# Optimization experiments

Measured on AMD Instinct MI355X. Metric: run time of the kernel, lower is better.

Reference implementation:

```python
import jax, jax.numpy as jnp
import numpy as np

HEAD_NUM = 16
HEAD_DIM = 64
INPUT_DIM = 1024
OUTPUT_DIM = 1024
NEG_INF = -1e9  # value the torch code writes into masked score positions


def setup_inputs() -> dict:
    key = jax.random.key(0)
    k_x, k_v, k_w1, k_b1, k_w2, k_b2 = jax.random.split(key, 6)
    B, N = 2, 2048
    x = jax.random.normal(k_x, (B, N, INPUT_DIM), dtype=jnp.float32)
    vaild_num = jax.random.randint(k_v, (B,), 0, N, dtype=jnp.int32)
    s1 = 1.0 / np.sqrt(INPUT_DIM)
    s2 = 1.0 / np.sqrt(HEAD_NUM * HEAD_DIM)
    W_qkv = jax.random.uniform(k_w1, (INPUT_DIM, 3 * HEAD_NUM * HEAD_DIM), jnp.float32, -s1, s1)
    b_qkv = jax.random.uniform(k_b1, (3 * HEAD_NUM * HEAD_DIM,), jnp.float32, -s1, s1)
    W_proj = jax.random.uniform(k_w2, (HEAD_NUM * HEAD_DIM, OUTPUT_DIM), jnp.float32, -s2, s2)
    b_proj = jax.random.uniform(k_b2, (OUTPUT_DIM,), jnp.float32, -s2, s2)
    return {"x": x, "vaild_num": vaild_num, "W_qkv": W_qkv, "b_qkv": b_qkv,
            "W_proj": W_proj, "b_proj": b_proj}


def reference(x, vaild_num, W_qkv, b_qkv, W_proj, b_proj):
    B, N, _ = x.shape
    H, hd = HEAD_NUM, HEAD_DIM
    qkv = x @ W_qkv + b_qkv                      # [B, N, 3*H*hd]
    q, k, v = jnp.split(qkv, 3, axis=2)
    split = lambda t: t.reshape(B, N, H, hd).transpose(0, 2, 1, 3)  # [B, H, N, hd]
    q, k, v = split(q), split(k), split(v)
    score = jnp.einsum('bhqd,bhkd->bhqk', q, k) * (1.0 / np.sqrt(hd))
    # per-sample valid-length masking: rows >= v and cols >= v get -1e9
    valid = jnp.arange(N)[None, :] < vaild_num[:, None]            # [B, N]
    mask = valid[:, None, :, None] & valid[:, None, None, :]       # [B, 1, N, N]
    score = jnp.where(mask, score, NEG_INF)
    p = jax.nn.softmax(score, axis=-1)
    attn = jnp.einsum('bhqk,bhkd->bhqd', p, v)                     # [B, H, N, hd]
    attn = attn.transpose(0, 2, 1, 3).reshape(B, N, H * hd)
    return attn @ W_proj + b_proj
```

## Files before the change

### kernel.cpp

```cpp
#include <hip/hip_runtime.h>
#include <stdint.h>


typedef float    f32x4  __attribute__((ext_vector_type(4)));
typedef float    f32x16 __attribute__((ext_vector_type(16)));
typedef __bf16   bf16x8 __attribute__((ext_vector_type(8)));
typedef unsigned short u16x8 __attribute__((ext_vector_type(8)));
typedef unsigned int   u32x4 __attribute__((ext_vector_type(4)));
typedef unsigned short ushort_t;
typedef unsigned int   u32;

#define HEADS 16
#define HDIM  64
#define NTOK  2048
#define BATCH 2
#define DIN   1024
#define D3    3072
#define MTOT  4096

#define SC 0.18033688f

__device__ __forceinline__ ushort_t f2bf(float x) {
  uint32_t u = __builtin_bit_cast(uint32_t, x);
  uint32_t r = (u + 0x7fffu + ((u >> 16) & 1u)) >> 16;
  return (ushort_t)r;
}
__device__ __forceinline__ float bf2f(ushort_t u) {
  return __builtin_bit_cast(float, (uint32_t)u << 16);
}
__device__ __forceinline__ u32 cvt_pk_bf16(float lo, float hi) {
  u32 r;
  asm("v_cvt_pk_bf16_f32 %0, %1, %2" : "=v"(r) : "v"(lo), "v"(hi));
  return r;
}

__device__ __forceinline__ void gld_lds16(const void* g, void* l) {
  auto gp = reinterpret_cast<const __attribute__((address_space(1))) uint32_t*>(
      reinterpret_cast<uintptr_t>(g));
  auto lp = reinterpret_cast<__attribute__((address_space(3))) uint32_t*>(
      reinterpret_cast<uintptr_t>(l));
  __builtin_amdgcn_global_load_lds(gp, lp, 16, 0, 0);
}

__device__ __forceinline__ void transpose_tile(
    const float* __restrict__ in, ushort_t* __restrict__ out,
    int R, int C, int bx, int by, float (*tile)[65]) {
  const int r0 = by * 64, c0 = bx * 64;
  const int t = threadIdx.x;
#pragma unroll
  for (int it = 0; it < 4; ++it) {
    int r = it * 16 + (t >> 4);
    int c = (t & 15) * 4;
    float4 v = *(const float4*)(in + (size_t)(r0 + r) * C + c0 + c);
    tile[r][c] = v.x; tile[r][c+1] = v.y; tile[r][c+2] = v.z; tile[r][c+3] = v.w;
  }
  __syncthreads();
#pragma unroll
  for (int it = 0; it < 2; ++it) {
    int idx = it * 2048 + t * 8;
    int c = idx >> 6;
    int r = idx & 63;
    u16x8 v;
#pragma unroll
    for (int j = 0; j < 8; ++j) v[j] = f2bf(tile[r + j][c]);
    *(u16x8*)(out + (size_t)(c0 + c) * R + r0 + r) = v;
  }
}

__global__ __launch_bounds__(256) void prep_kernel(
    const float* __restrict__ x, ushort_t* __restrict__ xb,
    const float* __restrict__ Wq, ushort_t* __restrict__ wqT,
    const float* __restrict__ Wp, ushort_t* __restrict__ wpT) {
  __shared__ float tile[64][65];
  const int bid = blockIdx.x;
  if (bid < 2048) {
    const int i = (bid * 256 + threadIdx.x) * 8;
    float4 a = *(const float4*)(x + i);
    float4 b = *(const float4*)(x + i + 4);
    u16x8 v;
    v[0]=f2bf(a.x); v[1]=f2bf(a.y); v[2]=f2bf(a.z); v[3]=f2bf(a.w);
    v[4]=f2bf(b.x); v[5]=f2bf(b.y); v[6]=f2bf(b.z); v[7]=f2bf(b.w);
    *(u16x8*)(xb + i) = v;
  } else if (bid < 2816) {
    const int idx = bid - 2048;
    transpose_tile(Wq, wqT, 1024, 3072, idx % 48, idx / 48, tile);
  } else {
    const int idx = bid - 2816;
    transpose_tile(Wp, wpT, 1024, 1024, idx % 16, idx / 16, tile);
  }
}

template <bool SWAP>
__device__ __forceinline__ void gemm_tile_mainloop(
    const ushort_t* __restrict__ A, const ushort_t* __restrict__ Bt,
    const int K, const int m0, const int n0,
    ushort_t* aT, ushort_t* bT, f32x4 (&acc)[4][4]) {
  const int t = threadIdx.x;
  const int l = t & 63;
  const int wr = t >> 7;
  const int wc = (t >> 6) & 1;

#pragma unroll
  for (int mi = 0; mi < 4; ++mi)
#pragma unroll
    for (int ni = 0; ni < 4; ++ni) acc[mi][ni] = f32x4{0.f, 0.f, 0.f, 0.f};

  for (int k0 = 0; k0 < K; k0 += 64) {
#pragma unroll
    for (int c = 0; c < 4; ++c) {
      const int lin = c * 4096 + t * 16;
      const int row = lin >> 7;
      const int scb = (lin & 127) ^ ((row & 7) << 4);
      const int ldso = (c * 4096 + (t >> 6) * 1024) >> 1;
      gld_lds16(A + (size_t)(m0 + row) * K + k0 + (scb >> 1), aT + ldso);
      gld_lds16(Bt + (size_t)(n0 + row) * K + k0 + (scb >> 1), bT + ldso);
    }
    __syncthreads();
#pragma unroll
    for (int ks = 0; ks < 2; ++ks) {
      bf16x8 af[4], bfr[4];
#pragma unroll
      for (int mi = 0; mi < 4; ++mi) {
        const int row = wr * 64 + mi * 16 + (l & 15);
        const int cb = (((l >> 4) << 4) + (ks << 6)) ^ ((row & 7) << 4);
        af[mi] = *(const bf16x8*)((const char*)aT + row * 128 + cb);
      }
#pragma unroll
      for (int ni = 0; ni < 4; ++ni) {
        const int row = wc * 64 + ni * 16 + (l & 15);
        const int cb = (((l >> 4) << 4) + (ks << 6)) ^ ((row & 7) << 4);
        bfr[ni] = *(const bf16x8*)((const char*)bT + row * 128 + cb);
      }
#pragma unroll
      for (int mi = 0; mi < 4; ++mi)
#pragma unroll
        for (int ni = 0; ni < 4; ++ni) {
          if (SWAP)
            acc[mi][ni] = __builtin_amdgcn_mfma_f32_16x16x32_bf16(
                bfr[ni], af[mi], acc[mi][ni], 0, 0, 0);
          else
            acc[mi][ni] = __builtin_amdgcn_mfma_f32_16x16x32_bf16(
                af[mi], bfr[ni], acc[mi][ni], 0, 0, 0);
        }
    }
    __syncthreads();
  }
}

__global__ __launch_bounds__(256) void gemm_qkv_kernel(
    const ushort_t* __restrict__ xb, const ushort_t* __restrict__ wT,
    const float* __restrict__ bias,
    ushort_t* __restrict__ Qb, ushort_t* __restrict__ Kb, ushort_t* __restrict__ Vt) {
  __shared__ __align__(16) ushort_t aT[128 * 64];
  __shared__ __align__(16) ushort_t bT[128 * 64];
  f32x4 acc[4][4];
  const int m0 = blockIdx.y * 128, n0 = blockIdx.x * 128;
  const int which = n0 >> 10;

  const int t = threadIdx.x, l = t & 63;
  const int wr = t >> 7, wc = (t >> 6) & 1;

  if (which != 2) {
    gemm_tile_mainloop<false>(xb, wT, DIN, m0, n0, aT, bT, acc);
#pragma unroll
    for (int mi = 0; mi < 4; ++mi) {
#pragma unroll
      for (int ni = 0; ni < 4; ++ni) {
        const int n = n0 + wc * 64 + ni * 16 + (l & 15);
        const int h = (n >> 6) & 15, d = n & 63;
        const float bv = bias[n];
#pragma unroll
        for (int i = 0; i < 4; ++i) {
          const int m = m0 + wr * 64 + mi * 16 + ((l >> 4) << 2) + i;
          const int b = m >> 11, tok = m & 2047;
          const ushort_t val = f2bf(acc[mi][ni][i] + bv);
          const size_t bh = (size_t)((b << 4) + h);
          if (which == 0) Qb[(bh * NTOK + tok) * HDIM + d] = val;
          else            Kb[(bh * NTOK + tok) * HDIM + d] = val;
        }
      }
    }
  } else {
    gemm_tile_mainloop<true>(xb, wT, DIN, m0, n0, aT, bT, acc);
    const int b = m0 >> 11;
    const int tok_base = (m0 & 2047) + wr * 64 + (l & 15);
    const int nd_base = (n0 - 2048) + wc * 64 + ((l >> 4) << 2);
#pragma unroll
    for (int mi = 0; mi < 4; ++mi) {
      const int tok = tok_base + mi * 16;
#pragma unroll
      for (int ni = 0; ni < 4; ++ni) {
#pragma unroll
        for (int i = 0; i < 4; ++i) {
          const int nd = nd_base + ni * 16 + i;
          const int h = nd >> 6, d = nd & 63;
          const float bv = bias[2048 + nd];
          Vt[(((size_t)((b << 4) + h) << 6) + d) * NTOK + tok] =
              f2bf(acc[mi][ni][i] + bv);
        }
      }
    }
  }
}

__global__ __launch_bounds__(256) void gemm_proj_kernel(
    const ushort_t* __restrict__ ab, const ushort_t* __restrict__ wT,
    const float* __restrict__ bias, float* __restrict__ out) {
  __shared__ __align__(16) ushort_t aT[128 * 64];
  __shared__ __align__(16) ushort_t bT[128 * 64];
  f32x4 acc[4][4];
  const int m0 = blockIdx.y * 128, n0 = blockIdx.x * 128;
  gemm_tile_mainloop<false>(ab, wT, DIN, m0, n0, aT, bT, acc);

  const int t = threadIdx.x, l = t & 63;
  const int wr = t >> 7, wc = (t >> 6) & 1;
#pragma unroll
  for (int mi = 0; mi < 4; ++mi) {
#pragma unroll
    for (int ni = 0; ni < 4; ++ni) {
      const int n = n0 + wc * 64 + ni * 16 + (l & 15);
      const float bv = bias[n];
#pragma unroll
      for (int i = 0; i < 4; ++i) {
        const int m = m0 + wr * 64 + mi * 16 + ((l >> 4) << 2) + i;
        out[(size_t)m * 1024 + n] = acc[mi][ni][i] + bv;
      }
    }
  }
}

__global__ __launch_bounds__(256) void vmean_kernel(
    const ushort_t* __restrict__ Vt, ushort_t* __restrict__ vmean) {
  const int row = blockIdx.x * 4 + (threadIdx.x >> 6);
  const int l = threadIdx.x & 63;
  const ushort_t* src = Vt + (size_t)row * NTOK;
  float s = 0.f;
#pragma unroll
  for (int j = 0; j < 4; ++j) {
    u16x8 v = *(const u16x8*)(src + ((j << 6) + l) * 8);
#pragma unroll
    for (int k = 0; k < 8; ++k) s += bf2f(v[k]);
  }
#pragma unroll
  for (int d2 = 1; d2 < 64; d2 <<= 1) s += __shfl_xor(s, d2);
  if (l == 0) vmean[row] = f2bf(s * (1.0f / 2048.0f));
}

__global__ __launch_bounds__(256) void attn_kernel(
    const ushort_t* __restrict__ Qb, const ushort_t* __restrict__ Kb,
    const ushort_t* __restrict__ Vt, const ushort_t* __restrict__ vmean,
    const int* __restrict__ validp, ushort_t* __restrict__ ob) {
  __shared__ __align__(16) char smem_raw[65536];

  const int h = blockIdx.y, b = blockIdx.z;
  const int valid = validp[b];
  const int t = threadIdx.x, w = t >> 6, l = t & 63;
  const int lq = l & 31, hi = l >> 5;
  const int bq0 = blockIdx.x << 7;
  const int wq0 = bq0 + (w << 5);
  const size_t bh = (size_t)((b << 4) + h);
  const ushort_t* Qp = Qb + bh * (NTOK * HDIM);
  const ushort_t* Kp = Kb + bh * (NTOK * HDIM);
  const ushort_t* Vp = Vt + bh * (HDIM * NTOK);

  f32x16 oacc[2];
#pragma unroll
  for (int db = 0; db < 2; ++db)
#pragma unroll
    for (int r = 0; r < 16; ++r) oacc[db][r] = 0.f;
  float m_run = -INFINITY, lsum = 0.f;

  if (bq0 < valid) {
    const bool qvalid = (wq0 < valid);
    bf16x8 qf[4];
    if (qvalid) {
      const ushort_t* qbase = Qp + (size_t)(wq0 + lq) * HDIM + (hi << 3);
#pragma unroll
      for (int ks = 0; ks < 4; ++ks) qf[ks] = *(const bf16x8*)(qbase + (ks << 4));
    }

    const int nt = (valid + 127) >> 7;

    auto STAGE = [&](int p, int kv0) {
      char* kdst = smem_raw + p * 32768;
      char* vdst = kdst + 16384;
#pragma unroll
      for (int c = 0; c < 4; ++c) {
        const int lin = c * 4096 + t * 16;
        const int ldso = c * 4096 + (w << 10);
        {
          const int row = lin >> 7;
          const int scb = (lin & 127) ^ ((row & 7) << 4);
          gld_lds16(Kp + (size_t)(kv0 + row) * HDIM + (scb >> 1), kdst + ldso);
        }
        {
          const int row = lin >> 8;
          const int scb = (lin & 255) ^ ((row & 7) << 4);
          gld_lds16(Vp + (size_t)row * NTOK + kv0 + (scb >> 1), vdst + ldso);
        }
      }
    };

    STAGE(0, 0);
    asm volatile("s_waitcnt vmcnt(0)" ::: "memory");
    __builtin_amdgcn_s_barrier();

    for (int tt = 0; tt < nt; ++tt) {
      const int p = tt & 1;
      const int kv0 = tt << 7;
      if (tt + 1 < nt) {
        STAGE(p ^ 1, (tt + 1) << 7);
        asm volatile("s_waitcnt vmcnt(8)" ::: "memory");
      } else {
        asm volatile("s_waitcnt vmcnt(0)" ::: "memory");
      }
      __builtin_amdgcn_sched_barrier(0);
      __builtin_amdgcn_s_barrier();

      if (qvalid) {
        const char* kbuf = smem_raw + p * 32768;
        const char* vbuf = kbuf + 16384;

        bf16x8 kf[4][4];
#pragma unroll
        for (int kb2 = 0; kb2 < 4; ++kb2) {
          const int row = (kb2 << 5) + lq;
          const int sw = (row & 7) << 4;
#pragma unroll
          for (int ks = 0; ks < 4; ++ks)
            kf[kb2][ks] = *(const bf16x8*)(kbuf + row * 128 + (((ks << 5) + (hi << 4)) ^ sw));
        }

        f32x16 st[4];
#pragma unroll
        for (int kb2 = 0; kb2 < 4; ++kb2)
#pragma unroll
          for (int r = 0; r < 16; ++r) st[kb2][r] = 0.f;
        __builtin_amdgcn_s_setprio(1);
#pragma unroll
        for (int ks = 0; ks < 4; ++ks) {
          st[0] = __builtin_amdgcn_mfma_f32_32x32x16_bf16(kf[0][ks], qf[ks], st[0], 0, 0, 0);
          st[1] = __builtin_amdgcn_mfma_f32_32x32x16_bf16(kf[1][ks], qf[ks], st[1], 0, 0, 0);
          st[2] = __builtin_amdgcn_mfma_f32_32x32x16_bf16(kf[2][ks], qf[ks], st[2], 0, 0, 0);
          st[3] = __builtin_amdgcn_mfma_f32_32x32x16_bf16(kf[3][ks], qf[ks], st[3], 0, 0, 0);
        }
        __builtin_amdgcn_s_setprio(0);

        if (kv0 + 128 > valid) {
#pragma unroll
          for (int kb2 = 0; kb2 < 4; ++kb2)
#pragma unroll
            for (int r = 0; r < 16; ++r) {
              const int k = kv0 + (kb2 << 5) + (r & 3) + ((r >> 2) << 3) + (hi << 2);
              if (k >= valid) st[kb2][r] = -1e30f;
            }
        }

        float pm;
        {
          float a8[8];
#pragma unroll
          for (int i = 0; i < 8; ++i)
            a8[i] = fmaxf(fmaxf(fmaxf(st[0][i], st[0][i + 8]), fmaxf(st[1][i], st[1][i + 8])),
                          fmaxf(fmaxf(st[2][i], st[2][i + 8]), fmaxf(st[3][i], st[3][i + 8])));
          float b4[4];
#pragma unroll
          for (int i = 0; i < 4; ++i) b4[i] = fmaxf(a8[i], a8[i + 4]);
          pm = fmaxf(fmaxf(b4[0], b4[1]), fmaxf(b4[2], b4[3]));
        }
        pm = fmaxf(pm, __shfl_xor(pm, 32));

        if (__any(pm > m_run)) {
          const float mnew = fmaxf(m_run, pm);
          const float rs = exp2f((m_run - mnew) * SC);
          lsum *= rs;
#pragma unroll
          for (int db = 0; db < 2; ++db)
#pragma unroll
            for (int r = 0; r < 16; ++r) oacc[db][r] *= rs;
          m_run = mnew;
        }

        const float mc = m_run * SC;
        float pp[4][16];
        float ts4[4] = {0.f, 0.f, 0.f, 0.f};
#pragma unroll
        for (int kb2 = 0; kb2 < 4; ++kb2)
#pragma unroll
          for (int r = 0; r < 16; ++r) {
            const float e = exp2f(fmaf(st[kb2][r], SC, -mc));
            pp[kb2][r] = e;
            ts4[r & 3] += e;
          }
        float tsum = (ts4[0] + ts4[1]) + (ts4[2] + ts4[3]);
        tsum += __shfl_xor(tsum, 32);
        lsum += tsum;

        bf16x8 pb[4][2];
#pragma unroll
        for (int kb2 = 0; kb2 < 4; ++kb2) {
          u32 c[8];
#pragma unroll
          for (int m2 = 0; m2 < 8; ++m2)
            c[m2] = cvt_pk_bf16(pp[kb2][2 * m2], pp[kb2][2 * m2 + 1]);
          const u32 x1 = (u32)__shfl_xor((int)(hi ? c[0] : c[2]), 32);
          const u32 x2 = (u32)__shfl_xor((int)(hi ? c[1] : c[3]), 32);
          const u32 x3 = (u32)__shfl_xor((int)(hi ? c[4] : c[6]), 32);
          const u32 x4 = (u32)__shfl_xor((int)(hi ? c[5] : c[7]), 32);
          u32x4 w0, w1;
          w0[0] = hi ? x1 : c[0];  w0[1] = hi ? x2 : c[1];
          w0[2] = hi ? c[2] : x1;  w0[3] = hi ? c[3] : x2;
          w1[0] = hi ? x3 : c[4];  w1[1] = hi ? x4 : c[5];
          w1[2] = hi ? c[6] : x3;  w1[3] = hi ? c[7] : x4;
          pb[kb2][0] = __builtin_bit_cast(bf16x8, w0);
          pb[kb2][1] = __builtin_bit_cast(bf16x8, w1);
        }

        __builtin_amdgcn_s_setprio(1);
#pragma unroll
        for (int db = 0; db < 2; ++db) {
          const int row = (db << 5) + lq;
          const int sw = (row & 7) << 4;
#pragma unroll
          for (int ksl = 0; ksl < 8; ++ksl) {
            const bf16x8 vf = *(const bf16x8*)(vbuf + row * 256 + (((ksl << 5) + (hi << 4)) ^ sw));
            oacc[db] = __builtin_amdgcn_mfma_f32_32x32x16_bf16(
                vf, pb[ksl >> 1][ksl & 1], oacc[db], 0, 0, 0);
          }
        }
        __builtin_amdgcn_s_setprio(0);
      }

      __builtin_amdgcn_s_barrier();
    }
  }

  const float inv = (lsum > 0.f) ? 1.0f / lsum : 0.f;
  ushort_t* ot = (ushort_t*)smem_raw + w * (32 * 68);
#pragma unroll
  for (int db = 0; db < 2; ++db)
#pragma unroll
    for (int r = 0; r < 16; ++r) {
      const int d = (r & 3) + ((r >> 2) << 3) + (hi << 2) + (db << 5);
      ot[lq * 68 + d] = f2bf(oacc[db][r] * inv);
    }
  asm volatile("s_waitcnt lgkmcnt(0)" ::: "memory");
#pragma unroll
  for (int it = 0; it < 8; ++it) {
    const int c2 = it * 64 + l;
    const int row = c2 >> 4;
    const int ch = c2 & 15;
    const uint2 vo = *(const uint2*)((const char*)ot + row * 136 + ch * 8);
    const uint2 vm = *(const uint2*)(vmean + (bh << 6) + ch * 4);
    const int grow = bq0 + (w << 5) + row;
    const uint2 sel = (grow < valid) ? vo : vm;
    *(uint2*)(ob + ((size_t)(b * NTOK) + grow) * 1024 + (h << 6) + ch * 4) = sel;
  }
}

extern "C" void kernel_launch(void* const* d_in, const int* in_sizes, int n_in,
                              void* d_out, int out_size, void* d_ws, size_t ws_size,
                              hipStream_t stream) {
  (void)in_sizes; (void)n_in; (void)out_size; (void)ws_size;
  const float* x      = (const float*)d_in[0];
  const int*   validp = (const int*)d_in[1];
  const float* W_qkv  = (const float*)d_in[2];
  const float* b_qkv  = (const float*)d_in[3];
  const float* W_proj = (const float*)d_in[4];
  const float* b_proj = (const float*)d_in[5];
  float* out = (float*)d_out;

  ushort_t* xb     = (ushort_t*)d_ws;
  ushort_t* wqkvT  = xb + 4194304;
  ushort_t* wprojT = wqkvT + 3145728;
  ushort_t* Qb     = wprojT + 1048576;
  ushort_t* Kb     = Qb + 4194304;
  ushort_t* Vt     = Kb + 4194304;
  ushort_t* ab     = Vt + 4194304;
  ushort_t* vm     = ab + 4194304;

  prep_kernel<<<3072, 256, 0, stream>>>(x, xb, W_qkv, wqkvT, W_proj, wprojT);
  gemm_qkv_kernel<<<dim3(24, 32), 256, 0, stream>>>(xb, wqkvT, b_qkv, Qb, Kb, Vt);
  vmean_kernel<<<512, 256, 0, stream>>>(Vt, vm);
  attn_kernel<<<dim3(16, 16, 2), 256, 0, stream>>>(Qb, Kb, Vt, vm, validp, ab);
  gemm_proj_kernel<<<dim3(8, 32), 256, 0, stream>>>(ab, wprojT, b_proj, out);
}
```

Baseline: 206.7 us.

## Split attention KV range across two blocks and merge partial results

The attention kernel now launches twice as many blocks. Each block processes alternating 128-key tiles (split-K, flash-decoding style) and writes bf16 partial outputs plus per-row max and sum to workspace. A new merge kernel combines the two partials with log-sum-exp rescaling and fills invalid rows with the V mean. This raises parallelism and occupancy for the attention stage, which had only 512 blocks with uneven valid lengths. The cost is an extra kernel launch, extra memory traffic for the partials, and bf16 rounding of the intermediate outputs.

```diff
diff --git a/kernel.cpp b/kernel.cpp
--- a/kernel.cpp
+++ b/kernel.cpp
@@ -248,21 +248,25 @@
 
 __global__ __launch_bounds__(256) void attn_kernel(
     const ushort_t* __restrict__ Qb, const ushort_t* __restrict__ Kb,
-    const ushort_t* __restrict__ Vt, const ushort_t* __restrict__ vmean,
-    const int* __restrict__ validp, ushort_t* __restrict__ ob) {
+    const ushort_t* __restrict__ Vt, const int* __restrict__ validp,
+    ushort_t* __restrict__ pO, float* __restrict__ pML) {
   __shared__ __align__(16) char smem_raw[65536];
 
+  const int qt = blockIdx.x & 15, half = blockIdx.x >> 4;
   const int h = blockIdx.y, b = blockIdx.z;
   const int valid = validp[b];
   const int t = threadIdx.x, w = t >> 6, l = t & 63;
   const int lq = l & 31, hi = l >> 5;
-  const int bq0 = blockIdx.x << 7;
+  const int bq0 = qt << 7;
   const int wq0 = bq0 + (w << 5);
   const size_t bh = (size_t)((b << 4) + h);
+  const int pidx = (int)((bh << 4) + qt) * 2 + half;
   const ushort_t* Qp = Qb + bh * (NTOK * HDIM);
   const ushort_t* Kp = Kb + bh * (NTOK * HDIM);
   const ushort_t* Vp = Vt + bh * (HDIM * NTOK);
 
+  if (bq0 >= valid) return;
+
   f32x16 oacc[2];
 #pragma unroll
   for (int db = 0; db < 2; ++db)
@@ -270,169 +274,170 @@
     for (int r = 0; r < 16; ++r) oacc[db][r] = 0.f;
   float m_run = -INFINITY, lsum = 0.f;
 
-  if (bq0 < valid) {
-    const bool qvalid = (wq0 < valid);
-    bf16x8 qf[4];
-    if (qvalid) {
-      const ushort_t* qbase = Qp + (size_t)(wq0 + lq) * HDIM + (hi << 3);
-#pragma unroll
-      for (int ks = 0; ks < 4; ++ks) qf[ks] = *(const bf16x8*)(qbase + (ks << 4));
-    }
-
-    const int nt = (valid + 127) >> 7;
-
-    auto STAGE = [&](int p, int kv0) {
-      char* kdst = smem_raw + p * 32768;
-      char* vdst = kdst + 16384;
-#pragma unroll
-      for (int c = 0; c < 4; ++c) {
-        const int lin = c * 4096 + t * 16;
-        const int ldso = c * 4096 + (w << 10);
-        {
-          const int row = lin >> 7;
-          const int scb = (lin & 127) ^ ((row & 7) << 4);
-          gld_lds16(Kp + (size_t)(kv0 + row) * HDIM + (scb >> 1), kdst + ldso);
-        }
-        {
-          const int row = lin >> 8;
-          const int scb = (lin & 255) ^ ((row & 7) << 4);
-          gld_lds16(Vp + (size_t)row * NTOK + kv0 + (scb >> 1), vdst + ldso);
-        }
-      }
-    };
-
-    STAGE(0, 0);
+  const bool qvalid = (wq0 < valid);
+  bf16x8 qf[4];
+  if (qvalid) {
+    const ushort_t* qbase = Qp + (size_t)(wq0 + lq) * HDIM + (hi << 3);
+#pragma unroll
+    for (int ks = 0; ks < 4; ++ks) qf[ks] = *(const bf16x8*)(qbase + (ks << 4));
+  }
+
+  const int nt = (valid + 127) >> 7;
+  const int ntb = (nt - half + 1) >> 1;
+
+  auto STAGE = [&](int p, int kv0) {
+    char* kdst = smem_raw + p * 32768;
+    char* vdst = kdst + 16384;
+#pragma unroll
+    for (int c = 0; c < 4; ++c) {
+      const int lin = c * 4096 + t * 16;
+      const int ldso = c * 4096 + (w << 10);
+      {
+        const int row = lin >> 7;
+        const int scb = (lin & 127) ^ ((row & 7) << 4);
+        gld_lds16(Kp + (size_t)(kv0 + row) * HDIM + (scb >> 1), kdst + ldso);
+      }
+      {
+        const int row = lin >> 8;
+        const int scb = (lin & 255) ^ ((row & 7) << 4);
+        gld_lds16(Vp + (size_t)row * NTOK + kv0 + (scb >> 1), vdst + ldso);
+      }
+    }
+  };
+
+  if (ntb > 0) {
+    STAGE(0, half << 7);
     asm volatile("s_waitcnt vmcnt(0)" ::: "memory");
     __builtin_amdgcn_s_barrier();
-
-    for (int tt = 0; tt < nt; ++tt) {
-      const int p = tt & 1;
-      const int kv0 = tt << 7;
-      if (tt + 1 < nt) {
-        STAGE(p ^ 1, (tt + 1) << 7);
-        asm volatile("s_waitcnt vmcnt(8)" ::: "memory");
-      } else {
-        asm volatile("s_waitcnt vmcnt(0)" ::: "memory");
-      }
-      __builtin_amdgcn_sched_barrier(0);
-      __builtin_amdgcn_s_barrier();
-
-      if (qvalid) {
-        const char* kbuf = smem_raw + p * 32768;
-        const char* vbuf = kbuf + 16384;
-
-        bf16x8 kf[4][4];
-#pragma unroll
-        for (int kb2 = 0; kb2 < 4; ++kb2) {
-          const int row = (kb2 << 5) + lq;
-          const int sw = (row & 7) << 4;
-#pragma unroll
-          for (int ks = 0; ks < 4; ++ks)
-            kf[kb2][ks] = *(const bf16x8*)(kbuf + row * 128 + (((ks << 5) + (hi << 4)) ^ sw));
+  }
+
+  for (int j = 0; j < ntb; ++j) {
+    const int p = j & 1;
+    const int kv0 = (half + 2 * j) << 7;
+    if (j + 1 < ntb) {
+      STAGE(p ^ 1, (half + 2 * (j + 1)) << 7);
+      asm volatile("s_waitcnt vmcnt(8)" ::: "memory");
+    } else {
+      asm volatile("s_waitcnt vmcnt(0)" ::: "memory");
+    }
+    __builtin_amdgcn_sched_barrier(0);
+    __builtin_amdgcn_s_barrier();
+
+    if (qvalid) {
+      const char* kbuf = smem_raw + p * 32768;
+      const char* vbuf = kbuf + 16384;
+
+      bf16x8 kf[4][4];
+#pragma unroll
+      for (int kb2 = 0; kb2 < 4; ++kb2) {
+        const int row = (kb2 << 5) + lq;
+        const int sw = (row & 7) << 4;
+#pragma unroll
+        for (int ks = 0; ks < 4; ++ks)
+          kf[kb2][ks] = *(const bf16x8*)(kbuf + row * 128 + (((ks << 5) + (hi << 4)) ^ sw));
+      }
+
+      f32x16 st[4];
+#pragma unroll
+      for (int kb2 = 0; kb2 < 4; ++kb2)
+#pragma unroll
+        for (int r = 0; r < 16; ++r) st[kb2][r] = 0.f;
+      __builtin_amdgcn_s_setprio(1);
+#pragma unroll
+      for (int ks = 0; ks < 4; ++ks) {
+        st[0] = __builtin_amdgcn_mfma_f32_32x32x16_bf16(kf[0][ks], qf[ks], st[0], 0, 0, 0);
+        st[1] = __builtin_amdgcn_mfma_f32_32x32x16_bf16(kf[1][ks], qf[ks], st[1], 0, 0, 0);
+        st[2] = __builtin_amdgcn_mfma_f32_32x32x16_bf16(kf[2][ks], qf[ks], st[2], 0, 0, 0);
+        st[3] = __builtin_amdgcn_mfma_f32_32x32x16_bf16(kf[3][ks], qf[ks], st[3], 0, 0, 0);
+      }
+      __builtin_amdgcn_s_setprio(0);
+
+      if (kv0 + 128 > valid) {
+#pragma unroll
+        for (int kb2 = 0; kb2 < 4; ++kb2)
+#pragma unroll
+          for (int r = 0; r < 16; ++r) {
+            const int k = kv0 + (kb2 << 5) + (r & 3) + ((r >> 2) << 3) + (hi << 2);
+            if (k >= valid) st[kb2][r] = -1e30f;
+          }
+      }
+
+      float pm;
+      {
+        float a8[8];
+#pragma unroll
+        for (int i = 0; i < 8; ++i)
+          a8[i] = fmaxf(fmaxf(fmaxf(st[0][i], st[0][i + 8]), fmaxf(st[1][i], st[1][i + 8])),
+                        fmaxf(fmaxf(st[2][i], st[2][i + 8]), fmaxf(st[3][i], st[3][i + 8])));
+        float b4[4];
+#pragma unroll
+        for (int i = 0; i < 4; ++i) b4[i] = fmaxf(a8[i], a8[i + 4]);
+        pm = fmaxf(fmaxf(b4[0], b4[1]), fmaxf(b4[2], b4[3]));
+      }
+      pm = fmaxf(pm, __shfl_xor(pm, 32));
+
+      if (__any(pm > m_run)) {
+        const float mnew = fmaxf(m_run, pm);
+        const float rs = exp2f((m_run - mnew) * SC);
+        lsum *= rs;
+#pragma unroll
+        for (int db = 0; db < 2; ++db)
+#pragma unroll
+          for (int r = 0; r < 16; ++r) oacc[db][r] *= rs;
+        m_run = mnew;
+      }
+
+      const float mc = m_run * SC;
+      float pp[4][16];
+      float ts4[4] = {0.f, 0.f, 0.f, 0.f};
+#pragma unroll
+      for (int kb2 = 0; kb2 < 4; ++kb2)
+#pragma unroll
+        for (int r = 0; r < 16; ++r) {
+          const float e = exp2f(fmaf(st[kb2][r], SC, -mc));
+          pp[kb2][r] = e;
+          ts4[r & 3] += e;
         }
-
-        f32x16 st[4];
-#pragma unroll
-        for (int kb2 = 0; kb2 < 4; ++kb2)
-#pragma unroll
-          for (int r = 0; r < 16; ++r) st[kb2][r] = 0.f;
-        __builtin_amdgcn_s_setprio(1);
-#pragma unroll
-        for (int ks = 0; ks < 4; ++ks) {
-          st[0] = __builtin_amdgcn_mfma_f32_32x32x16_bf16(kf[0][ks], qf[ks], st[0], 0, 0, 0);
-          st[1] = __builtin_amdgcn_mfma_f32_32x32x16_bf16(kf[1][ks], qf[ks], st[1], 0, 0, 0);
-          st[2] = __builtin_amdgcn_mfma_f32_32x32x16_bf16(kf[2][ks], qf[ks], st[2], 0, 0, 0);
-          st[3] = __builtin_amdgcn_mfma_f32_32x32x16_bf16(kf[3][ks], qf[ks], st[3], 0, 0, 0);
+      float tsum = (ts4[0] + ts4[1]) + (ts4[2] + ts4[3]);
+      tsum += __shfl_xor(tsum, 32);
+      lsum += tsum;
+
+      bf16x8 pb[4][2];
+#pragma unroll
+      for (int kb2 = 0; kb2 < 4; ++kb2) {
+        u32 c[8];
+#pragma unroll
+        for (int m2 = 0; m2 < 8; ++m2)
+          c[m2] = cvt_pk_bf16(pp[kb2][2 * m2], pp[kb2][2 * m2 + 1]);
+        const u32 x1 = (u32)__shfl_xor((int)(hi ? c[0] : c[2]), 32);
+        const u32 x2 = (u32)__shfl_xor((int)(hi ? c[1] : c[3]), 32);
+        const u32 x3 = (u32)__shfl_xor((int)(hi ? c[4] : c[6]), 32);
+        const u32 x4 = (u32)__shfl_xor((int)(hi ? c[5] : c[7]), 32);
+        u32x4 w0, w1;
+        w0[0] = hi ? x1 : c[0];  w0[1] = hi ? x2 : c[1];
+        w0[2] = hi ? c[2] : x1;  w0[3] = hi ? c[3] : x2;
+        w1[0] = hi ? x3 : c[4];  w1[1] = hi ? x4 : c[5];
+        w1[2] = hi ? c[6] : x3;  w1[3] = hi ? c[7] : x4;
+        pb[kb2][0] = __builtin_bit_cast(bf16x8, w0);
+        pb[kb2][1] = __builtin_bit_cast(bf16x8, w1);
+      }
+
+      __builtin_amdgcn_s_setprio(1);
+#pragma unroll
+      for (int db = 0; db < 2; ++db) {
+        const int row = (db << 5) + lq;
+        const int sw = (row & 7) << 4;
+#pragma unroll
+        for (int ksl = 0; ksl < 8; ++ksl) {
+          const bf16x8 vf = *(const bf16x8*)(vbuf + row * 256 + (((ksl << 5) + (hi << 4)) ^ sw));
+          oacc[db] = __builtin_amdgcn_mfma_f32_32x32x16_bf16(
+              vf, pb[ksl >> 1][ksl & 1], oacc[db], 0, 0, 0);
         }
-        __builtin_amdgcn_s_setprio(0);
-
-        if (kv0 + 128 > valid) {
-#pragma unroll
-          for (int kb2 = 0; kb2 < 4; ++kb2)
-#pragma unroll
-            for (int r = 0; r < 16; ++r) {
-              const int k = kv0 + (kb2 << 5) + (r & 3) + ((r >> 2) << 3) + (hi << 2);
-              if (k >= valid) st[kb2][r] = -1e30f;
-            }
-        }
-
-        float pm;
-        {
-          float a8[8];
-#pragma unroll
-          for (int i = 0; i < 8; ++i)
-            a8[i] = fmaxf(fmaxf(fmaxf(st[0][i], st[0][i + 8]), fmaxf(st[1][i], st[1][i + 8])),
-                          fmaxf(fmaxf(st[2][i], st[2][i + 8]), fmaxf(st[3][i], st[3][i + 8])));
-          float b4[4];
-#pragma unroll
-          for (int i = 0; i < 4; ++i) b4[i] = fmaxf(a8[i], a8[i + 4]);
-          pm = fmaxf(fmaxf(b4[0], b4[1]), fmaxf(b4[2], b4[3]));
-        }
-        pm = fmaxf(pm, __shfl_xor(pm, 32));
-
-        if (__any(pm > m_run)) {
-          const float mnew = fmaxf(m_run, pm);
-          const float rs = exp2f((m_run - mnew) * SC);
-          lsum *= rs;
-#pragma unroll
-          for (int db = 0; db < 2; ++db)
-#pragma unroll
-            for (int r = 0; r < 16; ++r) oacc[db][r] *= rs;
-          m_run = mnew;
-        }
-
-        const float mc = m_run * SC;
-        float pp[4][16];
-        float ts4[4] = {0.f, 0.f, 0.f, 0.f};
-#pragma unroll
-        for (int kb2 = 0; kb2 < 4; ++kb2)
-#pragma unroll
-          for (int r = 0; r < 16; ++r) {
-            const float e = exp2f(fmaf(st[kb2][r], SC, -mc));
-            pp[kb2][r] = e;
-            ts4[r & 3] += e;
-          }
-        float tsum = (ts4[0] + ts4[1]) + (ts4[2] + ts4[3]);
-        tsum += __shfl_xor(tsum, 32);
-        lsum += tsum;
-
-        bf16x8 pb[4][2];
-#pragma unroll
-        for (int kb2 = 0; kb2 < 4; ++kb2) {
-          u32 c[8];
-#pragma unroll
-          for (int m2 = 0; m2 < 8; ++m2)
-            c[m2] = cvt_pk_bf16(pp[kb2][2 * m2], pp[kb2][2 * m2 + 1]);
-          const u32 x1 = (u32)__shfl_xor((int)(hi ? c[0] : c[2]), 32);
-          const u32 x2 = (u32)__shfl_xor((int)(hi ? c[1] : c[3]), 32);
-          const u32 x3 = (u32)__shfl_xor((int)(hi ? c[4] : c[6]), 32);
-          const u32 x4 = (u32)__shfl_xor((int)(hi ? c[5] : c[7]), 32);
-          u32x4 w0, w1;
-          w0[0] = hi ? x1 : c[0];  w0[1] = hi ? x2 : c[1];
-          w0[2] = hi ? c[2] : x1;  w0[3] = hi ? c[3] : x2;
-          w1[0] = hi ? x3 : c[4];  w1[1] = hi ? x4 : c[5];
-          w1[2] = hi ? c[6] : x3;  w1[3] = hi ? c[7] : x4;
-          pb[kb2][0] = __builtin_bit_cast(bf16x8, w0);
-          pb[kb2][1] = __builtin_bit_cast(bf16x8, w1);
-        }
-
-        __builtin_amdgcn_s_setprio(1);
-#pragma unroll
-        for (int db = 0; db < 2; ++db) {
-          const int row = (db << 5) + lq;
-          const int sw = (row & 7) << 4;
-#pragma unroll
-          for (int ksl = 0; ksl < 8; ++ksl) {
-            const bf16x8 vf = *(const bf16x8*)(vbuf + row * 256 + (((ksl << 5) + (hi << 4)) ^ sw));
-            oacc[db] = __builtin_amdgcn_mfma_f32_32x32x16_bf16(
-                vf, pb[ksl >> 1][ksl & 1], oacc[db], 0, 0, 0);
-          }
-        }
-        __builtin_amdgcn_s_setprio(0);
-      }
-
-      __builtin_amdgcn_s_barrier();
-    }
+      }
+      __builtin_amdgcn_s_setprio(0);
+    }
+
+    __builtin_amdgcn_s_barrier();
   }
 
   const float inv = (lsum > 0.f) ? 1.0f / lsum : 0.f;
@@ -445,16 +450,62 @@
       ot[lq * 68 + d] = f2bf(oacc[db][r] * inv);
     }
   asm volatile("s_waitcnt lgkmcnt(0)" ::: "memory");
+  ushort_t* po = pO + (size_t)pidx * 8192;
 #pragma unroll
   for (int it = 0; it < 8; ++it) {
     const int c2 = it * 64 + l;
     const int row = c2 >> 4;
     const int ch = c2 & 15;
-    const uint2 vo = *(const uint2*)((const char*)ot + row * 136 + ch * 8);
-    const uint2 vm = *(const uint2*)(vmean + (bh << 6) + ch * 4);
-    const int grow = bq0 + (w << 5) + row;
-    const uint2 sel = (grow < valid) ? vo : vm;
-    *(uint2*)(ob + ((size_t)(b * NTOK) + grow) * 1024 + (h << 6) + ch * 4) = sel;
+    const uint2 vo = *(const uint2*)(ot + row * 68 + ch * 4);
+    *(uint2*)(po + (w * 32 + row) * 64 + ch * 4) = vo;
+  }
+  if (hi == 0) {
+    float* ml = pML + (size_t)pidx * 256 + (w * 32 + lq) * 2;
+    ml[0] = m_run;
+    ml[1] = lsum;
+  }
+}
+
+__global__ __launch_bounds__(256) void merge_kernel(
+    const ushort_t* __restrict__ pO, const float* __restrict__ pML,
+    const ushort_t* __restrict__ vmean, const int* __restrict__ validp,
+    ushort_t* __restrict__ ab) {
+  const int qt = blockIdx.x, h = blockIdx.y, b = blockIdx.z;
+  const int valid = validp[b];
+  const int bq0 = qt << 7;
+  const int t = threadIdx.x;
+  const size_t bh = (size_t)((b << 4) + h);
+  const int p0 = (int)((bh << 4) + qt) * 2;
+  const ushort_t* O0 = pO + (size_t)p0 * 8192;
+  const ushort_t* O1 = O0 + 8192;
+  const float* ML0 = pML + (size_t)p0 * 256;
+  const float* ML1 = ML0 + 256;
+
+#pragma unroll
+  for (int it = 0; it < 16; ++it) {
+    const int idx = it * 512 + t * 2;
+    const int row = idx >> 6;
+    const int d = idx & 63;
+    const int grow = bq0 + row;
+    u32 res;
+    if (grow < valid) {
+      const float m0 = ML0[row * 2], l0 = ML0[row * 2 + 1];
+      const float m1 = ML1[row * 2], l1 = ML1[row * 2 + 1];
+      const float M = fmaxf(m0, m1);
+      const float a0 = l0 * exp2f((m0 - M) * SC);
+      const float a1 = l1 * exp2f((m1 - M) * SC);
+      const float inv = 1.0f / (a0 + a1);
+      const u32 q0 = *(const u32*)(O0 + row * 64 + d);
+      const u32 q1 = *(const u32*)(O1 + row * 64 + d);
+      const float rlo = (bf2f((ushort_t)(q0 & 0xffff)) * a0 +
+                         bf2f((ushort_t)(q1 & 0xffff)) * a1) * inv;
+      const float rhi = (bf2f((ushort_t)(q0 >> 16)) * a0 +
+                         bf2f((ushort_t)(q1 >> 16)) * a1) * inv;
+      res = (u32)f2bf(rlo) | ((u32)f2bf(rhi) << 16);
+    } else {
+      res = *(const u32*)(vmean + (bh << 6) + d);
+    }
+    *(u32*)(ab + ((size_t)(b * NTOK) + grow) * 1024 + (h << 6) + d) = res;
   }
 }
 
@@ -470,18 +521,21 @@
   const float* b_proj = (const float*)d_in[5];
   float* out = (float*)d_out;
 
-  ushort_t* xb     = (ushort_t*)d_ws;
-  ushort_t* wqkvT  = xb + 4194304;
-  ushort_t* wprojT = wqkvT + 3145728;
+  ushort_t* wprojT = (ushort_t*)d_ws;
   ushort_t* Qb     = wprojT + 1048576;
   ushort_t* Kb     = Qb + 4194304;
   ushort_t* Vt     = Kb + 4194304;
   ushort_t* ab     = Vt + 4194304;
   ushort_t* vm     = ab + 4194304;
+  ushort_t* xb     = vm + 2048;
+  ushort_t* wqkvT  = xb + 4194304;
+  ushort_t* pO     = xb;
+  float*    pML    = (float*)(pO + 8388608);
 
   prep_kernel<<<3072, 256, 0, stream>>>(x, xb, W_qkv, wqkvT, W_proj, wprojT);
   gemm_qkv_kernel<<<dim3(24, 32), 256, 0, stream>>>(xb, wqkvT, b_qkv, Qb, Kb, Vt);
   vmean_kernel<<<512, 256, 0, stream>>>(Vt, vm);
-  attn_kernel<<<dim3(16, 16, 2), 256, 0, stream>>>(Qb, Kb, Vt, vm, validp, ab);
+  attn_kernel<<<dim3(32, 16, 2), 256, 0, stream>>>(Qb, Kb, Vt, validp, pO, pML);
+  merge_kernel<<<dim3(16, 16, 2), 256, 0, stream>>>(pO, pML, vm, validp, ab);
   gemm_proj_kernel<<<dim3(8, 32), 256, 0, stream>>>(ab, wprojT, b_proj, out);
 }
```

New measurement: 219.6 us. 1.06x slower.
